# Optimization experiments

Hardware: AMD Instinct MI355X
Metric: run time of the kernel (lower is better)

Reference implementation:

```python
import jax, jax.numpy as jnp
import numpy as np

NUM_ITER = 10
NUM_LAYER = 3
EMB_DIM = 128
ALPHA = 0.1
NUM_ATOM_FEATS = 9
ATOM_VOCAB = 119
N_NODES = 50000
N_EDGES = 800000


def setup_inputs() -> dict:
    key = jax.random.key(0)
    ks = jax.random.split(key, 5)
    x = jax.random.randint(ks[0], (N_NODES, NUM_ATOM_FEATS), 0, ATOM_VOCAB, dtype=jnp.int64 if jax.config.jax_enable_x64 else jnp.int32)
    edge_index = jax.random.randint(ks[1], (2, N_EDGES), 0, N_NODES, dtype=jnp.int32)
    scale = 1.0 / np.sqrt(EMB_DIM)
    atom_emb = jax.random.normal(ks[2], (NUM_ATOM_FEATS, ATOM_VOCAB, EMB_DIM), dtype=jnp.float32) * 0.1
    Ws = jax.random.normal(ks[3], (NUM_LAYER, EMB_DIM, EMB_DIM), dtype=jnp.float32) * scale
    bs = jax.random.normal(ks[4], (NUM_LAYER, EMB_DIM), dtype=jnp.float32) * 0.01
    return {"x": x, "edge_index": edge_index, "atom_emb": atom_emb, "Ws": Ws, "bs": bs}


def _forward(x, edge_index, atom_emb, Ws, bs):
    N = x.shape[0]
    # AtomEncoder: sum of per-feature-column embeddings -> [N, d]
    h = jax.vmap(lambda tbl, ids: tbl[ids], in_axes=(0, 1))(atom_emb, x).sum(axis=0)
    # MLP stack with ReLU on all but last layer
    L = Ws.shape[0]
    for l in range(L):
        h = h @ Ws[l] + bs[l]
        if l != L - 1:
            h = jax.nn.relu(h)
    # gcn_norm with self loops, unit edge weights (eval mode: no edge dropout)
    self_idx = jnp.arange(N, dtype=edge_index.dtype)
    src = jnp.concatenate([edge_index[0], self_idx])
    dst = jnp.concatenate([edge_index[1], self_idx])
    deg = jax.ops.segment_sum(jnp.ones(src.shape[0], dtype=h.dtype), dst, num_segments=N)
    dinv = jnp.where(deg > 0, jax.lax.rsqrt(jnp.maximum(deg, 1e-12)), 0.0)
    coef = (dinv[src] * dinv[dst])[:, None]  # [E+N, 1]
    h0 = h
    def body(i, h):
        agg = jax.ops.segment_sum(coef * h[src], dst, num_segments=N)
        return (1.0 - ALPHA) * agg + ALPHA * h0
    h = jax.lax.fori_loop(0, NUM_ITER, body, h)
    return h  # JK == 'last'


def reference(x, edge_index, atom_emb, Ws, bs):
    return _forward(x, edge_index, atom_emb, Ws, bs)
```

## Files before the change

### kernel.cpp

```cpp
#include <hip/hip_runtime.h>

#define N_NODES 50000
#define N_EDGES 800000
#define EMB 128
#define NFEAT 9
#define VOCAB 119
#define NITER 10
#define ALPHA 0.1f


__device__ inline unsigned int f2bf1(float x) {
    union { float f; unsigned u; } v; v.f = x;
    unsigned r = v.u + 0x7fffu + ((v.u >> 16) & 1u);
    return r >> 16;
}
__device__ inline unsigned int f2bf2(float lo, float hi) {
    return f2bf1(lo) | (f2bf1(hi) << 16);
}
__device__ inline float bf2f_lo(unsigned u) {
    union { unsigned u; float f; } v; v.u = u << 16; return v.f;
}
__device__ inline float bf2f_hi(unsigned u) {
    union { unsigned u; float f; } v; v.u = u & 0xffff0000u; return v.f;
}

struct __attribute__((aligned(4))) i4 { int x, y, z, w; };


__global__ void k_zero(int* __restrict__ cnt) {
    int i = blockIdx.x * blockDim.x + threadIdx.x;
    if (i < N_NODES) cnt[i] = 0;
}

__global__ void k_count(const int* __restrict__ dst, int* __restrict__ cnt,
                        int* __restrict__ ord) {
    int e = blockIdx.x * blockDim.x + threadIdx.x;
    if (e < N_EDGES) ord[e] = atomicAdd(&cnt[dst[e]], 1);
}

__global__ void k_scan1(const int* __restrict__ cnt, int* __restrict__ rowptr,
                        int* __restrict__ bsum, float* __restrict__ dinv) {
    __shared__ int s[256];
    int t = threadIdx.x;
    int idx = blockIdx.x * 256 + t;
    int v = (idx < N_NODES) ? cnt[idx] : 0;
    if (idx < N_NODES) dinv[idx] = rsqrtf((float)(v + 1));
    s[t] = v; __syncthreads();
    for (int off = 1; off < 256; off <<= 1) {
        int add = (t >= off) ? s[t - off] : 0;
        __syncthreads();
        s[t] += add;
        __syncthreads();
    }
    if (idx < N_NODES) rowptr[idx] = s[t] - v;
    if (t == 255) bsum[blockIdx.x] = s[255];
}

__global__ void k_scan2(int* __restrict__ bsum, int nb) {
    __shared__ int s[256];
    int t = threadIdx.x;
    int v = (t < nb) ? bsum[t] : 0;
    s[t] = v; __syncthreads();
    for (int off = 1; off < 256; off <<= 1) {
        int add = (t >= off) ? s[t - off] : 0;
        __syncthreads();
        s[t] += add;
        __syncthreads();
    }
    if (t < nb) bsum[t] = s[t] - v;
}

__global__ void k_scan3(int* __restrict__ rowptr, const int* __restrict__ bsum) {
    int idx = blockIdx.x * 256 + threadIdx.x;
    if (idx < N_NODES) rowptr[idx] += bsum[blockIdx.x];
}

__global__ void k_fill(const int* __restrict__ src, const int* __restrict__ dst,
                       const int* __restrict__ ord, const int* __restrict__ rowptr,
                       int* __restrict__ csr_src) {
    int e = blockIdx.x * blockDim.x + threadIdx.x;
    if (e < N_EDGES) {
        csr_src[rowptr[dst[e]] + ord[e]] = src[e];
    }
}


__global__ void k_encode(const int* __restrict__ x, const float* __restrict__ emb,
                         float* __restrict__ out) {
    int t = threadIdx.x;
    int d = t & 127, sub = t >> 7;
    int n = blockIdx.x * 2 + sub;
    if (n >= N_NODES) return;
    const int* xr = x + n * NFEAT;
    float s = 0.f;
#pragma unroll
    for (int f = 0; f < NFEAT; ++f) {
        int id = xr[f];
        s += emb[(f * VOCAB + id) * EMB + d];
    }
    out[n * EMB + d] = s;
}


__device__ inline void fma4(float4& acc, float4 a, float4 w0, float4 w1,
                            float4 w2, float4 w3) {
    acc.x = fmaf(a.x, w0.x, fmaf(a.y, w1.x, fmaf(a.z, w2.x, fmaf(a.w, w3.x, acc.x))));
    acc.y = fmaf(a.x, w0.y, fmaf(a.y, w1.y, fmaf(a.z, w2.y, fmaf(a.w, w3.y, acc.y))));
    acc.z = fmaf(a.x, w0.z, fmaf(a.y, w1.z, fmaf(a.z, w2.z, fmaf(a.w, w3.z, acc.z))));
    acc.w = fmaf(a.x, w0.w, fmaf(a.y, w1.w, fmaf(a.z, w2.w, fmaf(a.w, w3.w, acc.w))));
}

__device__ inline float4 relu4(float4 a) {
    return make_float4(fmaxf(a.x, 0.f), fmaxf(a.y, 0.f), fmaxf(a.z, 0.f), fmaxf(a.w, 0.f));
}

template <int RELU, int WQ>
__global__ __launch_bounds__(256) void k_mlp(const float* __restrict__ in,
                                             float* __restrict__ out,
                                             const float* __restrict__ W,
                                             const float* __restrict__ b,
                                             const float* __restrict__ dinv,
                                             uint2* __restrict__ q0out,
                                             uint2* __restrict__ h0bout) {
    __shared__ float4 hs[32 * 32];
    int t = threadIdx.x;
    int base = blockIdx.x * 32;
    const float4* in4 = (const float4*)in;
    for (int i = t; i < 32 * 32; i += 256) {
        int n = base + (i >> 5);
        hs[i] = (n < N_NODES) ? in4[n * 32 + (i & 31)] : make_float4(0.f, 0.f, 0.f, 0.f);
    }
    __syncthreads();
    int q = t & 31;
    int g = t >> 5;
    const float4* Wq = (const float4*)W + q;
    float4 bias = ((const float4*)b)[q];
    float4 acc0 = bias, acc1 = bias, acc2 = bias, acc3 = bias;
    const float4* h0r = &hs[(g * 4 + 0) * 32];
    const float4* h1r = &hs[(g * 4 + 1) * 32];
    const float4* h2r = &hs[(g * 4 + 2) * 32];
    const float4* h3r = &hs[(g * 4 + 3) * 32];
#pragma unroll 2
    for (int k0 = 0; k0 < EMB; k0 += 4) {
        float4 w0 = Wq[(k0 + 0) * 32];
        float4 w1 = Wq[(k0 + 1) * 32];
        float4 w2 = Wq[(k0 + 2) * 32];
        float4 w3 = Wq[(k0 + 3) * 32];
        int kq = k0 >> 2;
        fma4(acc0, h0r[kq], w0, w1, w2, w3);
        fma4(acc1, h1r[kq], w0, w1, w2, w3);
        fma4(acc2, h2r[kq], w0, w1, w2, w3);
        fma4(acc3, h3r[kq], w0, w1, w2, w3);
    }
    if (RELU) {
        acc0 = relu4(acc0); acc1 = relu4(acc1);
        acc2 = relu4(acc2); acc3 = relu4(acc3);
    }
    float4* out4 = (float4*)out;
    int n0 = base + g * 4;
    if (n0 + 0 < N_NODES) out4[(n0 + 0) * 32 + q] = acc0;
    if (n0 + 1 < N_NODES) out4[(n0 + 1) * 32 + q] = acc1;
    if (n0 + 2 < N_NODES) out4[(n0 + 2) * 32 + q] = acc2;
    if (n0 + 3 < N_NODES) out4[(n0 + 3) * 32 + q] = acc3;
    if (WQ) {
#pragma unroll
        for (int j = 0; j < 4; ++j) {
            int n = n0 + j;
            if (n < N_NODES) {
                float4 a = (j == 0) ? acc0 : (j == 1) ? acc1 : (j == 2) ? acc2 : acc3;
                float s = dinv[n];
                q0out[n * 32 + q] =
                    make_uint2(f2bf2(a.x * s, a.y * s), f2bf2(a.z * s, a.w * s));
                h0bout[n * 32 + q] =
                    make_uint2(f2bf2(a.x, a.y), f2bf2(a.z, a.w));
            }
        }
    }
}


#define ACC8(g) \
    a0 += bf2f_lo((g).x); a1 += bf2f_hi((g).x); \
    a2 += bf2f_lo((g).y); a3 += bf2f_hi((g).y); \
    a4 += bf2f_lo((g).z); a5 += bf2f_hi((g).z); \
    a6 += bf2f_lo((g).w); a7 += bf2f_hi((g).w);

#define SEL(iv) (pair == 0 ? (iv).x : pair == 1 ? (iv).y : pair == 2 ? (iv).z : (iv).w)

template <int LAST>
__global__ __launch_bounds__(256) void k_prop(const uint4* __restrict__ qin,
                                              const float4* __restrict__ h0,
                                              const uint4* __restrict__ h0b,
                                              void* __restrict__ outb,
                                              const int* __restrict__ rowptr,
                                              const int* __restrict__ cnt,
                                              const int* __restrict__ csr_src,
                                              const float* __restrict__ dinv) {
    int t = threadIdx.x;
    int lane = t & 63;
    int pair = lane >> 4;
    int dq = lane & 15;
    int v = blockIdx.x * 4 + (t >> 6);
    int start = __builtin_amdgcn_readfirstlane(rowptr[v]);
    int c = __builtin_amdgcn_readfirstlane(cnt[v]);
    const int* cs = csr_src + start;

    float dv = dinv[v];
    uint4 qv = qin[v * 16 + dq];
    float4 hlo, hhi; uint4 hvb;
    if (LAST) {
        hlo = h0[v * 32 + 2 * dq];
        hhi = h0[v * 32 + 2 * dq + 1];
    } else {
        hvb = h0b[v * 16 + dq];
    }

    float a0 = 0.f, a1 = 0.f, a2 = 0.f, a3 = 0.f;
    float a4 = 0.f, a5 = 0.f, a6 = 0.f, a7 = 0.f;
    int i = 0;
    for (; i + 32 <= c; i += 32) {
        i4 ia = *(const i4*)(cs + i);
        i4 ib = *(const i4*)(cs + i + 4);
        i4 ic = *(const i4*)(cs + i + 8);
        i4 id = *(const i4*)(cs + i + 12);
        i4 ie = *(const i4*)(cs + i + 16);
        i4 ifq = *(const i4*)(cs + i + 20);
        i4 ig = *(const i4*)(cs + i + 24);
        i4 ih = *(const i4*)(cs + i + 28);
        int s0 = SEL(ia), s1 = SEL(ib), s2 = SEL(ic), s3 = SEL(id);
        int s4 = SEL(ie), s5 = SEL(ifq), s6 = SEL(ig), s7 = SEL(ih);
        uint4 g0 = qin[s0 * 16 + dq];
        uint4 g1 = qin[s1 * 16 + dq];
        uint4 g2 = qin[s2 * 16 + dq];
        uint4 g3 = qin[s3 * 16 + dq];
        uint4 g4 = qin[s4 * 16 + dq];
        uint4 g5 = qin[s5 * 16 + dq];
        uint4 g6 = qin[s6 * 16 + dq];
        uint4 g7 = qin[s7 * 16 + dq];
        ACC8(g0); ACC8(g1); ACC8(g2); ACC8(g3);
        ACC8(g4); ACC8(g5); ACC8(g6); ACC8(g7);
    }
    for (; i + 8 <= c; i += 8) {
        i4 ia = *(const i4*)(cs + i);
        i4 ib = *(const i4*)(cs + i + 4);
        int s0 = SEL(ia), s1 = SEL(ib);
        uint4 g0 = qin[s0 * 16 + dq];
        uint4 g1 = qin[s1 * 16 + dq];
        ACC8(g0); ACC8(g1);
    }
    for (; i < c; i += 4) {
        int e = i + pair;
        if (e < c) {
            uint4 g = qin[cs[e] * 16 + dq];
            ACC8(g);
        }
    }
    a0 += __shfl_xor(a0, 16); a0 += __shfl_xor(a0, 32);
    a1 += __shfl_xor(a1, 16); a1 += __shfl_xor(a1, 32);
    a2 += __shfl_xor(a2, 16); a2 += __shfl_xor(a2, 32);
    a3 += __shfl_xor(a3, 16); a3 += __shfl_xor(a3, 32);
    a4 += __shfl_xor(a4, 16); a4 += __shfl_xor(a4, 32);
    a5 += __shfl_xor(a5, 16); a5 += __shfl_xor(a5, 32);
    a6 += __shfl_xor(a6, 16); a6 += __shfl_xor(a6, 32);
    a7 += __shfl_xor(a7, 16); a7 += __shfl_xor(a7, 32);

    float s0 = a0 + bf2f_lo(qv.x), s1 = a1 + bf2f_hi(qv.x);
    float s2 = a2 + bf2f_lo(qv.y), s3 = a3 + bf2f_hi(qv.y);
    float s4 = a4 + bf2f_lo(qv.z), s5 = a5 + bf2f_hi(qv.z);
    float s6 = a6 + bf2f_lo(qv.w), s7 = a7 + bf2f_hi(qv.w);
    const float K = 1.f - ALPHA;

    if (LAST) {
        float h_0 = K * dv * s0 + ALPHA * hlo.x;
        float h_1 = K * dv * s1 + ALPHA * hlo.y;
        float h_2 = K * dv * s2 + ALPHA * hlo.z;
        float h_3 = K * dv * s3 + ALPHA * hlo.w;
        float h_4 = K * dv * s4 + ALPHA * hhi.x;
        float h_5 = K * dv * s5 + ALPHA * hhi.y;
        float h_6 = K * dv * s6 + ALPHA * hhi.z;
        float h_7 = K * dv * s7 + ALPHA * hhi.w;
        if (pair < 2) {
            float4 wv = (pair == 0) ? make_float4(h_0, h_1, h_2, h_3)
                                    : make_float4(h_4, h_5, h_6, h_7);
            ((float4*)outb)[v * 32 + 2 * dq + pair] = wv;
        }
    } else {
        float h_0 = K * dv * s0 + ALPHA * bf2f_lo(hvb.x);
        float h_1 = K * dv * s1 + ALPHA * bf2f_hi(hvb.x);
        float h_2 = K * dv * s2 + ALPHA * bf2f_lo(hvb.y);
        float h_3 = K * dv * s3 + ALPHA * bf2f_hi(hvb.y);
        float h_4 = K * dv * s4 + ALPHA * bf2f_lo(hvb.z);
        float h_5 = K * dv * s5 + ALPHA * bf2f_hi(hvb.z);
        float h_6 = K * dv * s6 + ALPHA * bf2f_lo(hvb.w);
        float h_7 = K * dv * s7 + ALPHA * bf2f_hi(hvb.w);
        if (pair == 0) {
            uint4 wv;
            wv.x = f2bf2(h_0 * dv, h_1 * dv);
            wv.y = f2bf2(h_2 * dv, h_3 * dv);
            wv.z = f2bf2(h_4 * dv, h_5 * dv);
            wv.w = f2bf2(h_6 * dv, h_7 * dv);
            ((uint4*)outb)[v * 16 + dq] = wv;
        }
    }
}


extern "C" void kernel_launch(void* const* d_in, const int* in_sizes, int n_in,
                              void* d_out, int out_size, void* d_ws, size_t ws_size,
                              hipStream_t stream) {
    const int*   x    = (const int*)d_in[0];
    const int*   ei   = (const int*)d_in[1];
    const float* emb  = (const float*)d_in[2];
    const float* Ws   = (const float*)d_in[3];
    const float* bs   = (const float*)d_in[4];
    float* out = (float*)d_out;

    const int* src = ei;
    const int* dst = ei + N_EDGES;

    char* w = (char*)d_ws;
    size_t off = 0;
    auto alloc = [&](size_t bytes) {
        void* p = w + off;
        off += (bytes + 255) & ~(size_t)255;
        return p;
    };
    float* h0      = (float*)alloc((size_t)N_NODES * EMB * 4);
    float* hT      = (float*)alloc((size_t)N_NODES * EMB * 4);
    void*  qA      = alloc((size_t)N_NODES * EMB * 2);
    void*  qB      = alloc((size_t)N_NODES * EMB * 2);
    void*  h0b     = alloc((size_t)N_NODES * EMB * 2);
    float* dinv    = (float*)alloc(N_NODES * 4);
    int*   cnt     = (int*)alloc(N_NODES * 4);
    int*   rowptr  = (int*)alloc(N_NODES * 4);
    int*   bsum    = (int*)alloc(256 * 4);
    int*   csr_src = (int*)alloc(N_EDGES * 4);
    int*   ord     = (int*)alloc(N_EDGES * 4);
    (void)ws_size; (void)n_in; (void)in_sizes; (void)out_size;

    const int NB_N  = (N_NODES + 255) / 256;
    const int NB_E  = (N_EDGES + 255) / 256;
    const int NB_2N = (N_NODES + 1) / 2;
    const int NB_M  = (N_NODES + 31) / 32;
    const int NB_P  = N_NODES / 4;

    k_zero<<<NB_N, 256, 0, stream>>>(cnt);
    k_count<<<NB_E, 256, 0, stream>>>(dst, cnt, ord);
    k_scan1<<<NB_N, 256, 0, stream>>>(cnt, rowptr, bsum, dinv);
    k_scan2<<<1, 256, 0, stream>>>(bsum, NB_N);
    k_scan3<<<NB_N, 256, 0, stream>>>(rowptr, bsum);
    k_fill<<<NB_E, 256, 0, stream>>>(src, dst, ord, rowptr, csr_src);

    k_encode<<<NB_2N, 256, 0, stream>>>(x, emb, hT);
    k_mlp<1, 0><<<NB_M, 256, 0, stream>>>(hT, hT, Ws + 0 * EMB * EMB, bs + 0 * EMB,
                                          nullptr, nullptr, nullptr);
    k_mlp<1, 0><<<NB_M, 256, 0, stream>>>(hT, hT, Ws + 1 * EMB * EMB, bs + 1 * EMB,
                                          nullptr, nullptr, nullptr);
    k_mlp<0, 1><<<NB_M, 256, 0, stream>>>(hT, h0, Ws + 2 * EMB * EMB, bs + 2 * EMB,
                                          dinv, (uint2*)qA, (uint2*)h0b);

    const uint4* qin = (const uint4*)qA;
    for (int i = 0; i < NITER; ++i) {
        if (i == NITER - 1) {
            k_prop<1><<<NB_P, 256, 0, stream>>>(qin, (const float4*)h0,
                                                (const uint4*)h0b, out,
                                                rowptr, cnt, csr_src, dinv);
        } else {
            void* qo = (i & 1) ? qA : qB;
            k_prop<0><<<NB_P, 256, 0, stream>>>(qin, (const float4*)h0,
                                                (const uint4*)h0b, qo,
                                                rowptr, cnt, csr_src, dinv);
            qin = (const uint4*)qo;
        }
    }
}
```

Measured before the change: 584.5 us.

## Run MLP layers on bf16 MFMA with bf16 activations and transposed weights

```diff
diff --git a/kernel.cpp b/kernel.cpp
--- a/kernel.cpp
+++ b/kernel.cpp
@@ -1,12 +1,16 @@
 #include <hip/hip_runtime.h>
 
 #define N_NODES 50000
+#define NPAD    50048
 #define N_EDGES 800000
 #define EMB 128
 #define NFEAT 9
 #define VOCAB 119
 #define NITER 10
 #define ALPHA 0.1f
+
+typedef __attribute__((ext_vector_type(8))) short bf16x8;
+typedef __attribute__((ext_vector_type(4))) float f32x4;
 
 
 __device__ inline unsigned int f2bf1(float x) {
@@ -85,94 +89,93 @@
 }
 
 
+__global__ void k_wprep(const float* __restrict__ W, ushort* __restrict__ WT) {
+    int l = blockIdx.x >> 7;
+    int n = blockIdx.x & 127;
+    int k = threadIdx.x;
+    WT[(l * 128 + n) * 128 + k] = (ushort)f2bf1(W[(l * 128 + k) * 128 + n]);
+}
+
+
 __global__ void k_encode(const int* __restrict__ x, const float* __restrict__ emb,
-                         float* __restrict__ out) {
-    int t = threadIdx.x;
-    int d = t & 127, sub = t >> 7;
-    int n = blockIdx.x * 2 + sub;
-    if (n >= N_NODES) return;
+                         unsigned* __restrict__ hb) {
+    int t = threadIdx.x;
+    int sub = t >> 6;
+    int dq = t & 63;
+    int n = blockIdx.x * 4 + sub;
     const int* xr = x + n * NFEAT;
-    float s = 0.f;
+    float s0 = 0.f, s1 = 0.f;
 #pragma unroll
     for (int f = 0; f < NFEAT; ++f) {
-        int id = xr[f];
-        s += emb[(f * VOCAB + id) * EMB + d];
-    }
-    out[n * EMB + d] = s;
-}
-
-
-__device__ inline void fma4(float4& acc, float4 a, float4 w0, float4 w1,
-                            float4 w2, float4 w3) {
-    acc.x = fmaf(a.x, w0.x, fmaf(a.y, w1.x, fmaf(a.z, w2.x, fmaf(a.w, w3.x, acc.x))));
-    acc.y = fmaf(a.x, w0.y, fmaf(a.y, w1.y, fmaf(a.z, w2.y, fmaf(a.w, w3.y, acc.y))));
-    acc.z = fmaf(a.x, w0.z, fmaf(a.y, w1.z, fmaf(a.z, w2.z, fmaf(a.w, w3.z, acc.z))));
-    acc.w = fmaf(a.x, w0.w, fmaf(a.y, w1.w, fmaf(a.z, w2.w, fmaf(a.w, w3.w, acc.w))));
-}
-
-__device__ inline float4 relu4(float4 a) {
-    return make_float4(fmaxf(a.x, 0.f), fmaxf(a.y, 0.f), fmaxf(a.z, 0.f), fmaxf(a.w, 0.f));
-}
+        const float2 e = *(const float2*)&emb[(f * VOCAB + xr[f]) * EMB + 2 * dq];
+        s0 += e.x; s1 += e.y;
+    }
+    hb[n * 64 + dq] = f2bf2(s0, s1);
+}
+
 
 template <int RELU, int WQ>
-__global__ __launch_bounds__(256) void k_mlp(const float* __restrict__ in,
-                                             float* __restrict__ out,
-                                             const float* __restrict__ W,
-                                             const float* __restrict__ b,
-                                             const float* __restrict__ dinv,
-                                             uint2* __restrict__ q0out,
-                                             uint2* __restrict__ h0bout) {
-    __shared__ float4 hs[32 * 32];
-    int t = threadIdx.x;
-    int base = blockIdx.x * 32;
-    const float4* in4 = (const float4*)in;
-    for (int i = t; i < 32 * 32; i += 256) {
-        int n = base + (i >> 5);
-        hs[i] = (n < N_NODES) ? in4[n * 32 + (i & 31)] : make_float4(0.f, 0.f, 0.f, 0.f);
-    }
-    __syncthreads();
-    int q = t & 31;
-    int g = t >> 5;
-    const float4* Wq = (const float4*)W + q;
-    float4 bias = ((const float4*)b)[q];
-    float4 acc0 = bias, acc1 = bias, acc2 = bias, acc3 = bias;
-    const float4* h0r = &hs[(g * 4 + 0) * 32];
-    const float4* h1r = &hs[(g * 4 + 1) * 32];
-    const float4* h2r = &hs[(g * 4 + 2) * 32];
-    const float4* h3r = &hs[(g * 4 + 3) * 32];
-#pragma unroll 2
-    for (int k0 = 0; k0 < EMB; k0 += 4) {
-        float4 w0 = Wq[(k0 + 0) * 32];
-        float4 w1 = Wq[(k0 + 1) * 32];
-        float4 w2 = Wq[(k0 + 2) * 32];
-        float4 w3 = Wq[(k0 + 3) * 32];
-        int kq = k0 >> 2;
-        fma4(acc0, h0r[kq], w0, w1, w2, w3);
-        fma4(acc1, h1r[kq], w0, w1, w2, w3);
-        fma4(acc2, h2r[kq], w0, w1, w2, w3);
-        fma4(acc3, h3r[kq], w0, w1, w2, w3);
-    }
-    if (RELU) {
-        acc0 = relu4(acc0); acc1 = relu4(acc1);
-        acc2 = relu4(acc2); acc3 = relu4(acc3);
-    }
-    float4* out4 = (float4*)out;
-    int n0 = base + g * 4;
-    if (n0 + 0 < N_NODES) out4[(n0 + 0) * 32 + q] = acc0;
-    if (n0 + 1 < N_NODES) out4[(n0 + 1) * 32 + q] = acc1;
-    if (n0 + 2 < N_NODES) out4[(n0 + 2) * 32 + q] = acc2;
-    if (n0 + 3 < N_NODES) out4[(n0 + 3) * 32 + q] = acc3;
+__global__ __launch_bounds__(256) void k_mlp_mfma(
+        const uint4* __restrict__ inb,
+        uint4* __restrict__ outb,
+        const uint4* __restrict__ WT4,
+        const float* __restrict__ bias,
+        const float* __restrict__ dinv,
+        float* __restrict__ h0out,
+        ushort* __restrict__ q0out,
+        ushort* __restrict__ h0bout) {
+    int t = threadIdx.x;
+    int w = t >> 6;
+    int l = t & 63;
+    int lr = l & 15;
+    int kg = l >> 4;
+    int base = blockIdx.x * 64 + w * 16;
+    union U { uint4 u; bf16x8 b; };
+
+    int arow = base + lr;
+    bf16x8 afrag[4];
+#pragma unroll
+    for (int kc = 0; kc < 4; ++kc) {
+        U cu; cu.u = inb[arow * 16 + kc * 4 + kg];
+        afrag[kc] = cu.b;
+    }
+
+    f32x4 acc[8];
+#pragma unroll
+    for (int nt = 0; nt < 8; ++nt) {
+        float bv = bias[nt * 16 + lr];
+        acc[nt] = (f32x4){bv, bv, bv, bv};
+    }
+
+#pragma unroll
+    for (int kc = 0; kc < 4; ++kc) {
+#pragma unroll
+        for (int nt = 0; nt < 8; ++nt) {
+            U cu; cu.u = WT4[(nt * 16 + lr) * 16 + kc * 4 + kg];
+            acc[nt] = __builtin_amdgcn_mfma_f32_16x16x32_bf16(afrag[kc], cu.b,
+                                                              acc[nt], 0, 0, 0);
+        }
+    }
+
+    int orow = base + kg * 4;
+    float dv[4];
     if (WQ) {
 #pragma unroll
-        for (int j = 0; j < 4; ++j) {
-            int n = n0 + j;
-            if (n < N_NODES) {
-                float4 a = (j == 0) ? acc0 : (j == 1) ? acc1 : (j == 2) ? acc2 : acc3;
-                float s = dinv[n];
-                q0out[n * 32 + q] =
-                    make_uint2(f2bf2(a.x * s, a.y * s), f2bf2(a.z * s, a.w * s));
-                h0bout[n * 32 + q] =
-                    make_uint2(f2bf2(a.x, a.y), f2bf2(a.z, a.w));
+        for (int r = 0; r < 4; ++r) dv[r] = dinv[orow + r];
+    }
+#pragma unroll
+    for (int nt = 0; nt < 8; ++nt) {
+        int n = nt * 16 + lr;
+#pragma unroll
+        for (int r = 0; r < 4; ++r) {
+            float val = acc[nt][r];
+            if (RELU) val = fmaxf(val, 0.f);
+            if (WQ) {
+                h0out[(orow + r) * 128 + n] = val;
+                q0out[(orow + r) * 128 + n] = (ushort)f2bf1(val * dv[r]);
+                h0bout[(orow + r) * 128 + n] = (ushort)f2bf1(val);
+            } else {
+                ((ushort*)outb)[(orow + r) * 128 + n] = (ushort)f2bf1(val);
             }
         }
     }
@@ -325,23 +328,24 @@
         off += (bytes + 255) & ~(size_t)255;
         return p;
     };
-    float* h0      = (float*)alloc((size_t)N_NODES * EMB * 4);
-    float* hT      = (float*)alloc((size_t)N_NODES * EMB * 4);
-    void*  qA      = alloc((size_t)N_NODES * EMB * 2);
-    void*  qB      = alloc((size_t)N_NODES * EMB * 2);
-    void*  h0b     = alloc((size_t)N_NODES * EMB * 2);
-    float* dinv    = (float*)alloc(N_NODES * 4);
-    int*   cnt     = (int*)alloc(N_NODES * 4);
-    int*   rowptr  = (int*)alloc(N_NODES * 4);
-    int*   bsum    = (int*)alloc(256 * 4);
-    int*   csr_src = (int*)alloc(N_EDGES * 4);
-    int*   ord     = (int*)alloc(N_EDGES * 4);
+    float*  h0      = (float*)alloc((size_t)NPAD * EMB * 4);
+    void*   hb      = alloc((size_t)NPAD * EMB * 2);
+    void*   qA      = alloc((size_t)NPAD * EMB * 2);
+    void*   qB      = alloc((size_t)NPAD * EMB * 2);
+    void*   h0b     = alloc((size_t)NPAD * EMB * 2);
+    ushort* WT      = (ushort*)alloc((size_t)3 * 128 * 128 * 2);
+    float*  dinv    = (float*)alloc((size_t)NPAD * 4);
+    int*    cnt     = (int*)alloc(N_NODES * 4);
+    int*    rowptr  = (int*)alloc(N_NODES * 4);
+    int*    bsum    = (int*)alloc(256 * 4);
+    int*    csr_src = (int*)alloc(N_EDGES * 4);
+    int*    ord     = (int*)alloc(N_EDGES * 4);
     (void)ws_size; (void)n_in; (void)in_sizes; (void)out_size;
 
     const int NB_N  = (N_NODES + 255) / 256;
     const int NB_E  = (N_EDGES + 255) / 256;
-    const int NB_2N = (N_NODES + 1) / 2;
-    const int NB_M  = (N_NODES + 31) / 32;
+    const int NB_EN = N_NODES / 4;
+    const int NB_M  = NPAD / 64;
     const int NB_P  = N_NODES / 4;
 
     k_zero<<<NB_N, 256, 0, stream>>>(cnt);
@@ -351,13 +355,17 @@
     k_scan3<<<NB_N, 256, 0, stream>>>(rowptr, bsum);
     k_fill<<<NB_E, 256, 0, stream>>>(src, dst, ord, rowptr, csr_src);
 
-    k_encode<<<NB_2N, 256, 0, stream>>>(x, emb, hT);
-    k_mlp<1, 0><<<NB_M, 256, 0, stream>>>(hT, hT, Ws + 0 * EMB * EMB, bs + 0 * EMB,
-                                          nullptr, nullptr, nullptr);
-    k_mlp<1, 0><<<NB_M, 256, 0, stream>>>(hT, hT, Ws + 1 * EMB * EMB, bs + 1 * EMB,
-                                          nullptr, nullptr, nullptr);
-    k_mlp<0, 1><<<NB_M, 256, 0, stream>>>(hT, h0, Ws + 2 * EMB * EMB, bs + 2 * EMB,
-                                          dinv, (uint2*)qA, (uint2*)h0b);
+    k_wprep<<<384, 128, 0, stream>>>(Ws, WT);
+    k_encode<<<NB_EN, 256, 0, stream>>>(x, emb, (unsigned*)hb);
+    k_mlp_mfma<1, 0><<<NB_M, 256, 0, stream>>>(
+        (const uint4*)hb, (uint4*)hb, (const uint4*)(WT + 0 * 128 * 128),
+        bs + 0 * EMB, nullptr, nullptr, nullptr, nullptr);
+    k_mlp_mfma<1, 0><<<NB_M, 256, 0, stream>>>(
+        (const uint4*)hb, (uint4*)hb, (const uint4*)(WT + 1 * 128 * 128),
+        bs + 1 * EMB, nullptr, nullptr, nullptr, nullptr);
+    k_mlp_mfma<0, 1><<<NB_M, 256, 0, stream>>>(
+        (const uint4*)hb, nullptr, (const uint4*)(WT + 2 * 128 * 128),
+        bs + 2 * EMB, dinv, h0, (ushort*)qA, (ushort*)h0b);
 
     const uint4* qin = (const uint4*)qA;
     for (int i = 0; i < NITER; ++i) {
```

New measurement: 554.0 us. -5.2%, faster.
